# Optimization experiments

Measured on AMD Instinct MI355X. Metric: run time of the kernel, lower is better.

## Reference

```python
import jax, jax.numpy as jnp
import numpy as np

N = 4096
F_IN = 3000
F_OUT = 64
NEG_INF = jnp.float32(-9e15)


def _xavier(key, shape):
    fan_in, fan_out = shape[0], shape[-1]
    limit = (6.0 / (fan_in + fan_out)) ** 0.5
    return jax.random.uniform(key, shape, jnp.float32, -limit, limit)


def setup_inputs() -> dict:
    key = jax.random.key(0)
    ks = jax.random.split(key, 20)
    feat = jax.random.normal(ks[0], (N, F_IN), jnp.float32)
    feat_a = jax.random.normal(ks[1], (N, F_IN), jnp.float32)
    eye = jnp.eye(N, dtype=jnp.float32)
    adj = jnp.maximum((jax.random.uniform(ks[2], (N, N)) < 0.008).astype(jnp.float32), eye)
    graph_neigh = jnp.maximum((jax.random.uniform(ks[3], (N, N)) < 0.008).astype(jnp.float32), eye)
    return {
        "feat": feat,
        "feat_a": feat_a,
        "adj": adj,
        "graph_neigh": graph_neigh,
        "weight1": _xavier(ks[4], (F_IN, F_OUT)),
        "weight2": _xavier(ks[5], (F_OUT, F_IN)),
        "att_W": _xavier(ks[6], (F_OUT, F_OUT)),
        "a_src": _xavier(ks[7], (F_OUT, 1)),
        "a_dst": _xavier(ks[8], (F_OUT, 1)),
        "mlp_W1": _xavier(ks[9], (F_OUT, 256)),
        "mlp_b1": jnp.zeros((256,), jnp.float32),
        "mlp_W2": _xavier(ks[10], (256, 128)),
        "mlp_b2": jnp.zeros((128,), jnp.float32),
        "mlp_W3": _xavier(ks[11], (128, F_OUT)),
        "mlp_b3": jnp.zeros((F_OUT,), jnp.float32),
        "dmlp_W1": _xavier(ks[12], (F_OUT, 128)),
        "dmlp_b1": jnp.zeros((128,), jnp.float32),
        "dmlp_W2": _xavier(ks[13], (128, F_OUT)),
        "dmlp_b2": jnp.zeros((F_OUT,), jnp.float32),
        "bil_W": _xavier(ks[14], (F_OUT, F_OUT)),
        "bil_b": jnp.zeros((1,), jnp.float32),
    }


def reference(feat, feat_a, adj, graph_neigh,
              weight1, weight2, att_W, a_src, a_dst,
              mlp_W1, mlp_b1, mlp_W2, mlp_b2, mlp_W3, mlp_b3,
              dmlp_W1, dmlp_b1, dmlp_W2, dmlp_b2, bil_W, bil_b):
    relu = jax.nn.relu

    def attention(h):
        Wh = h @ att_W                      # [N, F_OUT]
        e = Wh @ a_src + (Wh @ a_dst).T     # [N, N]
        e = jnp.where(e > 0, e, 0.2 * e)    # LeakyReLU(0.2)
        e = jnp.where(adj > 0, e, NEG_INF)  # mask non-edges
        return jax.nn.softmax(e, axis=1) @ Wh

    def mlp(x):
        x = relu(x @ mlp_W1 + mlp_b1)
        x = relu(x @ mlp_W2 + mlp_b2)
        return x @ mlp_W3 + mlp_b3

    def dmlp(x):  # discriminator MLP: n_h -> 128 -> n_h
        return relu(x @ dmlp_W1 + dmlp_b1) @ dmlp_W2 + dmlp_b2

    def readout(emb):  # AvgReadout + L2 normalize
        g = (graph_neigh @ emb) / jnp.sum(graph_neigh, axis=1, keepdims=True)
        return g / jnp.maximum(jnp.linalg.norm(g, axis=1, keepdims=True), 1e-12)

    def bilinear(x, y):  # nn.Bilinear(n_h, n_h, 1)
        return (jnp.einsum('ni,ij,nj->n', x, bil_W, y) + bil_b)[:, None]

    def disc(c, h_pl, h_mi):
        c, h_pl, h_mi = dmlp(c), dmlp(h_pl), dmlp(h_mi)
        return jnp.concatenate([bilinear(h_pl, c), bilinear(h_mi, c)], axis=1)

    z = mlp(attention(feat @ weight1))
    hiden_emb = z
    h = adj @ (z @ weight2)                 # spmm(adj, z @ weight2)
    emb = relu(z)
    z_a = mlp(attention(feat_a @ weight1))
    emb_a = relu(z_a)
    g = jax.nn.sigmoid(readout(emb))
    g_a = jax.nn.sigmoid(readout(emb_a))
    ret = disc(g, emb, emb_a)
    ret_a = disc(g_a, emb_a, emb)
    return (hiden_emb, h, ret, ret_a)
```

## Files before the change

kernel.cpp:

```cpp
#include <hip/hip_runtime.h>

#define NN   4096
#define FIN  3000
#define MAXN 128

typedef unsigned short u16;
typedef __bf16 bf16x8 __attribute__((ext_vector_type(8)));
typedef float f32x16 __attribute__((ext_vector_type(16)));

__device__ __forceinline__ float bf2f(u16 u) { union { unsigned int i; float f; } v; v.i = ((unsigned int)u) << 16; return v.f; }
__device__ __forceinline__ u16 f2bf(float f) {
    union { float f; unsigned int i; } v; v.f = f;
    return (u16)((v.i + 0x7FFFu + ((v.i >> 16) & 1u)) >> 16);
}
__device__ __forceinline__ bf16x8 bzero8() {
    union { unsigned long long q[2]; bf16x8 v; } u; u.q[0] = 0ull; u.q[1] = 0ull; return u.v;
}
__device__ __forceinline__ f32x16 fzero16() {
    f32x16 v;
    #pragma unroll
    for (int i = 0; i < 16; i++) v[i] = 0.f;
    return v;
}

__global__ __launch_bounds__(1024) void k_detect(const u16* __restrict__ feat, int* __restrict__ flag)
{
    __shared__ int tot;
    if (threadIdx.x == 0) tot = 0;
    __syncthreads();
    int ins = 0;
    for (int i = threadIdx.x; i < 16384; i += 1024) {
        u16 u = feat[i];
        int e = (u >> 7) & 0xFF;
        if (u != 0 && (e < 90 || e > 160)) ins++;
    }
    atomicAdd(&tot, ins);
    __syncthreads();
    if (threadIdx.x == 0) *flag = (tot > 1024) ? 1 : 0;
}

__global__ __launch_bounds__(256) void k_convw(const int* __restrict__ flag,
    const void* s0, const void* s1, const void* s2, const void* s3,
    const void* s4, const void* s5, const void* s6, const void* s7,
    const void* s8, const void* s9, const void* s10, const void* s11,
    const void* s12, const void* s13, const void* s14, const void* s15,
    float* __restrict__ dst)
{
    const void* srcs[16] = {s0,s1,s2,s3,s4,s5,s6,s7,s8,s9,s10,s11,s12,s13,s14,s15};
    const int offs[16] = {0,192000,196096,196160,196224,212608,212864,245632,245760,253952,254016,262208,262336,270528,270592,274688};
    const int ns[16]   = {192000,4096,64,64,16384,256,32768,128,8192,64,8192,128,8192,64,4096,1};
    int seg = blockIdx.y;
    int i = blockIdx.x * 256 + threadIdx.x;
    if (i >= ns[seg]) return;
    float v = (*flag) ? ((const float*)srcs[seg])[i] : bf2f(((const u16*)srcs[seg])[i]);
    dst[offs[seg] + i] = v;
}

__global__ __launch_bounds__(256) void k_convw2t(const int* __restrict__ flag,
    const void* __restrict__ src, u16* __restrict__ WH, u16* __restrict__ WL)
{
    int i = blockIdx.x * 256 + threadIdx.x;
    if (i >= 3008 * 64) return;
    int n = i >> 6, k = i & 63;
    float v = 0.f;
    if (n < FIN)
        v = (*flag) ? ((const float*)src)[(size_t)k * FIN + n]
                    : bf2f(((const u16*)src)[(size_t)k * FIN + n]);
    u16 h = f2bf(v);
    float r = v - bf2f(h);
    WH[i] = h;
    WL[i] = f2bf(r);
}

__global__ __launch_bounds__(256) void k_convw1t(const int* __restrict__ flag,
    const void* __restrict__ w1src, u16* __restrict__ BtH, u16* __restrict__ BtL)
{
    int i = blockIdx.x * 256 + threadIdx.x;
    if (i >= 64 * 3008) return;
    int c = i / 3008, k = i - c * 3008;
    float v = 0.f;
    if (k < 3000)
        v = (*flag) ? ((const float*)w1src)[(size_t)k * 64 + c]
                    : bf2f(((const u16*)w1src)[(size_t)k * 64 + c]);
    u16 h = f2bf(v);
    float r = v - bf2f(h);
    BtH[(size_t)c * 3008 + k] = h;
    BtL[(size_t)c * 3008 + k] = f2bf(r);
}

__global__ __launch_bounds__(256) void k_build_csr(const int* __restrict__ flag,
    const void* __restrict__ Av, const void* __restrict__ Gv,
    int* __restrict__ aCnt, int* __restrict__ aIdx,
    int* __restrict__ gCnt, int* __restrict__ gIdx)
{
    bool isf = (*flag != 0);
    const void* M = blockIdx.y ? Gv : Av;
    int* cnt = blockIdx.y ? gCnt : aCnt;
    int* idx = blockIdx.y ? gIdx : aIdx;
    int row = blockIdx.x, t = threadIdx.x;
    int c0 = t * 16;
    unsigned int mask = 0; int my = 0;
    if (isf) {
        const float4* r = (const float4*)((const float*)M + (size_t)row * NN + c0);
        union { float4 q[4]; float f[16]; } u;
        u.q[0] = r[0]; u.q[1] = r[1]; u.q[2] = r[2]; u.q[3] = r[3];
        #pragma unroll
        for (int j = 0; j < 16; j++) if (u.f[j] != 0.f) { mask |= 1u << j; my++; }
    } else {
        const uint4* r = (const uint4*)((const u16*)M + (size_t)row * NN + c0);
        union { uint4 q[2]; u16 h[16]; } u;
        u.q[0] = r[0]; u.q[1] = r[1];
        #pragma unroll
        for (int j = 0; j < 16; j++) if (u.h[j] != 0) { mask |= 1u << j; my++; }
    }
    __shared__ int sc[256];
    sc[t] = my;
    __syncthreads();
    for (int d = 1; d < 256; d <<= 1) {
        int v = (t >= d) ? sc[t - d] : 0;
        __syncthreads();
        sc[t] += v;
        __syncthreads();
    }
    int pos = sc[t] - my;
    for (int j = 0; j < 16; j++) {
        if (mask & (1u << j)) {
            if (pos < MAXN) idx[(size_t)row * MAXN + pos] = c0 + j;
            pos++;
        }
    }
    if (t == 0) { int total = sc[255]; cnt[row] = (total < MAXN) ? total : MAXN; }
}

__global__ __launch_bounds__(512) void k_featgemm_mfma(const int* __restrict__ flag,
    const void* __restrict__ F0v, const void* __restrict__ F1v,
    const u16* __restrict__ BtH, float* __restrict__ X0, float* __restrict__ X1)
{
    if (*flag) return;
    const u16* F = (const u16*)(blockIdx.y ? F1v : F0v);
    float* X = blockIdx.y ? X1 : X0;
    int r0 = blockIdx.x * 32;
    int tid = threadIdx.x;
    int w  = tid >> 6;
    int l  = tid & 63;
    int lr = l & 31;
    int kg = l >> 5;
    const u16* arow = F   + (size_t)(r0 + lr) * FIN + kg * 8;
    const u16* b0p  = BtH + (size_t)lr * 3008 + kg * 8;
    const u16* b1p  = BtH + (size_t)(lr + 32) * 3008 + kg * 8;
    f32x16 acc0 = fzero16(), acc1 = fzero16();
    #pragma unroll 4
    for (int s = w; s < 188; s += 8) {
        int kk = s * 16;
        bf16x8 a;
        if (kk + kg * 8 < FIN) a = *(const bf16x8*)(arow + kk);
        else                   a = bzero8();
        bf16x8 b0 = *(const bf16x8*)(b0p + kk);
        bf16x8 b1 = *(const bf16x8*)(b1p + kk);
        acc0 = __builtin_amdgcn_mfma_f32_32x32x16_bf16(a, b0, acc0, 0, 0, 0);
        acc1 = __builtin_amdgcn_mfma_f32_32x32x16_bf16(a, b1, acc1, 0, 0, 0);
    }
    __shared__ float red[8][2048];
    float* rp = red[w];
    #pragma unroll
    for (int reg = 0; reg < 16; reg++) {
        int row = (reg & 3) + 8 * (reg >> 2) + 4 * kg;
        rp[row * 64 + lr] = acc0[reg];
    }
    #pragma unroll
    for (int reg = 0; reg < 16; reg++) {
        int row = (reg & 3) + 8 * (reg >> 2) + 4 * kg;
        rp[row * 64 + 32 + lr] = acc1[reg];
    }
    __syncthreads();
    for (int i = tid; i < 2048; i += 512) {
        float s0 = 0.f;
        #pragma unroll
        for (int j = 0; j < 8; j++) s0 += red[j][i];
        X[(size_t)r0 * 64 + i] = s0;
    }
}

__device__ __forceinline__ void fg_issue(
    const float* __restrict__ arow,
    const u16* __restrict__ b0h, const u16* __restrict__ b1h,
    const u16* __restrict__ b0l, const u16* __restrict__ b1l,
    int s, int kg,
    float4& A0, float4& A1, bf16x8& H0, bf16x8& H1, bf16x8& L0, bf16x8& L1)
{
    if (s < 188) {
        int kk = s * 16;
        if (kk + kg * 8 < FIN) {
            A0 = *(const float4*)(arow + kk);
            A1 = *(const float4*)(arow + kk + 4);
        } else {
            A0 = make_float4(0.f, 0.f, 0.f, 0.f);
            A1 = make_float4(0.f, 0.f, 0.f, 0.f);
        }
        H0 = *(const bf16x8*)(b0h + kk);
        H1 = *(const bf16x8*)(b1h + kk);
        L0 = *(const bf16x8*)(b0l + kk);
        L1 = *(const bf16x8*)(b1l + kk);
    } else {
        A0 = make_float4(0.f, 0.f, 0.f, 0.f);
        A1 = make_float4(0.f, 0.f, 0.f, 0.f);
        H0 = bzero8(); H1 = bzero8(); L0 = bzero8(); L1 = bzero8();
    }
}

__device__ __forceinline__ void fg_step(
    const float4& A0, const float4& A1,
    const bf16x8& H0, const bf16x8& H1, const bf16x8& L0, const bf16x8& L1,
    f32x16& acc0, f32x16& acc1)
{
    float av[8] = {A0.x, A0.y, A0.z, A0.w, A1.x, A1.y, A1.z, A1.w};
    bf16x8 ah, al;
    #pragma unroll
    for (int j = 0; j < 8; j++) {
        __bf16 hv = (__bf16)av[j];
        ah[j] = hv;
        al[j] = (__bf16)(av[j] - (float)hv);
    }
    acc0 = __builtin_amdgcn_mfma_f32_32x32x16_bf16(ah, H0, acc0, 0, 0, 0);
    acc0 = __builtin_amdgcn_mfma_f32_32x32x16_bf16(al, H0, acc0, 0, 0, 0);
    acc0 = __builtin_amdgcn_mfma_f32_32x32x16_bf16(ah, L0, acc0, 0, 0, 0);
    acc1 = __builtin_amdgcn_mfma_f32_32x32x16_bf16(ah, H1, acc1, 0, 0, 0);
    acc1 = __builtin_amdgcn_mfma_f32_32x32x16_bf16(al, H1, acc1, 0, 0, 0);
    acc1 = __builtin_amdgcn_mfma_f32_32x32x16_bf16(ah, L1, acc1, 0, 0, 0);
}

__global__ __launch_bounds__(512) void k_featgemm_mfma_f32(const int* __restrict__ flag,
    const void* __restrict__ F0v, const void* __restrict__ F1v,
    const u16* __restrict__ BtH, const u16* __restrict__ BtL,
    float* __restrict__ X0, float* __restrict__ X1)
{
    if (!*flag) return;
    const float* F = (const float*)(blockIdx.y ? F1v : F0v);
    float* X = blockIdx.y ? X1 : X0;
    int r0 = blockIdx.x * 32;
    int tid = threadIdx.x;
    int w  = tid >> 6;
    int l  = tid & 63;
    int lr = l & 31;
    int kg = l >> 5;
    int s0 = blockIdx.z * 8 + w;
    const float* arow = F + (size_t)(r0 + lr) * FIN + kg * 8;
    const u16* b0h = BtH + (size_t)lr * 3008 + kg * 8;
    const u16* b1h = BtH + (size_t)(lr + 32) * 3008 + kg * 8;
    const u16* b0l = BtL + (size_t)lr * 3008 + kg * 8;
    const u16* b1l = BtL + (size_t)(lr + 32) * 3008 + kg * 8;

    float4 A0[2], A1[2];
    bf16x8 H0[2], H1[2], L0[2], L1[2];
    fg_issue(arow, b0h, b1h, b0l, b1l, s0,      kg, A0[0], A1[0], H0[0], H1[0], L0[0], L1[0]);
    fg_issue(arow, b0h, b1h, b0l, b1l, s0 + 16, kg, A0[1], A1[1], H0[1], H1[1], L0[1], L1[1]);
    f32x16 acc0 = fzero16(), acc1 = fzero16();
    #pragma unroll
    for (int si = 0; si < 12; si++) {
        int sl = si & 1;
        fg_step(A0[sl], A1[sl], H0[sl], H1[sl], L0[sl], L1[sl], acc0, acc1);
        if (si + 2 < 12)
            fg_issue(arow, b0h, b1h, b0l, b1l, s0 + (si + 2) * 16, kg,
                     A0[sl], A1[sl], H0[sl], H1[sl], L0[sl], L1[sl]);
    }

    __shared__ float red[8][2048];
    float* rp = red[w];
    #pragma unroll
    for (int reg = 0; reg < 16; reg++) {
        int row = (reg & 3) + 8 * (reg >> 2) + 4 * kg;
        rp[row * 64 + lr] = acc0[reg];
    }
    #pragma unroll
    for (int reg = 0; reg < 16; reg++) {
        int row = (reg & 3) + 8 * (reg >> 2) + 4 * kg;
        rp[row * 64 + 32 + lr] = acc1[reg];
    }
    __syncthreads();
    for (int i = tid; i < 2048; i += 512) {
        float s0s = 0.f;
        #pragma unroll
        for (int j = 0; j < 8; j++) s0s += red[j][i];
        atomicAdd(&X[(size_t)r0 * 64 + i], s0s);
    }
}

__global__ __launch_bounds__(64) void k_whsd(
    const float* __restrict__ X1, const float* __restrict__ X2,
    const float* __restrict__ AW, const float* __restrict__ asrc, const float* __restrict__ adst,
    float* __restrict__ Wh1, float* __restrict__ Wh2,
    float* __restrict__ s1, float* __restrict__ s2,
    float* __restrict__ d1, float* __restrict__ d2)
{
    const float* X = blockIdx.y ? X2 : X1;
    float* Wh = blockIdx.y ? Wh2 : Wh1;
    float* sv = blockIdx.y ? s2 : s1;
    float* dv = blockIdx.y ? d2 : d1;
    int row = blockIdx.x, c = threadIdx.x;
    __shared__ float x[64];
    x[c] = X[(size_t)row * 64 + c];
    __syncthreads();
    float acc = 0.f;
    #pragma unroll 16
    for (int k = 0; k < 64; k++) acc += x[k] * AW[k * 64 + c];
    Wh[(size_t)row * 64 + c] = acc;
    float vs = acc * asrc[c];
    float vd = acc * adst[c];
    #pragma unroll
    for (int off = 32; off > 0; off >>= 1) { vs += __shfl_down(vs, off); vd += __shfl_down(vd, off); }
    if (c == 0) { sv[row] = vs; dv[row] = vd; }
}

__global__ __launch_bounds__(128) void k_attn(
    const int* __restrict__ cnt, const int* __restrict__ idx,
    const float* __restrict__ s1, const float* __restrict__ s2,
    const float* __restrict__ d1, const float* __restrict__ d2,
    const float* __restrict__ Wh1, const float* __restrict__ Wh2,
    float* __restrict__ A1, float* __restrict__ A2)
{
    const float* sp = blockIdx.y ? s2 : s1;
    const float* dp = blockIdx.y ? d2 : d1;
    const float* Wh = blockIdx.y ? Wh2 : Wh1;
    float* A = blockIdx.y ? A2 : A1;
    int row = blockIdx.x, tid = threadIdx.x;
    int n = cnt[row];
    __shared__ int js[MAXN];
    __shared__ float ps[MAXN];
    __shared__ float red2[2];
    __shared__ float ared[2][64];
    for (int k = tid; k < n; k += 128) js[k] = idx[(size_t)row * MAXN + k];
    __syncthreads();
    float si = sp[row];
    float m = -3.0e38f;
    for (int k = tid; k < n; k += 128) {
        float e = si + dp[js[k]];
        e = e > 0.f ? e : 0.2f * e;
        ps[k] = e;
        m = fmaxf(m, e);
    }
    #pragma unroll
    for (int off = 32; off > 0; off >>= 1) m = fmaxf(m, __shfl_down(m, off));
    if ((tid & 63) == 0) red2[tid >> 6] = m;
    __syncthreads();
    m = fmaxf(red2[0], red2[1]);
    __syncthreads();
    float zz = 0.f;
    for (int k = tid; k < n; k += 128) {
        float p = __expf(ps[k] - m);
        ps[k] = p;
        zz += p;
    }
    #pragma unroll
    for (int off = 32; off > 0; off >>= 1) zz += __shfl_down(zz, off);
    if ((tid & 63) == 0) red2[tid >> 6] = zz;
    __syncthreads();
    float Z = red2[0] + red2[1];
    Z = fmaxf(Z, 1e-20f);
    int f = tid & 63, half = tid >> 6;
    float acc = 0.f;
    for (int k = half; k < n; k += 2) acc += ps[k] * Wh[(size_t)js[k] * 64 + f];
    ared[half][f] = acc;
    __syncthreads();
    if (tid < 64) A[(size_t)row * 64 + f] = (ared[0][f] + ared[1][f]) / Z;
}

__global__ __launch_bounds__(256) void k_mlp(const int* __restrict__ flag,
    const float* __restrict__ A1, const float* __restrict__ A2,
    const float* __restrict__ W1, const float* __restrict__ b1,
    const float* __restrict__ W2, const float* __restrict__ b2,
    const float* __restrict__ W3, const float* __restrict__ b3,
    float* __restrict__ Z1, float* __restrict__ Z2, void* __restrict__ hidenv)
{
    const float* A = blockIdx.y ? A2 : A1;
    float* Z = blockIdx.y ? Z2 : Z1;
    int row0 = blockIdx.x * 4, tid = threadIdx.x;
    __shared__ float x[4][64], h1[4][256], h2[4][128];
    {
        int r = tid >> 6, c = tid & 63;
        x[r][c] = A[(size_t)(row0 + r) * 64 + c];
    }
    __syncthreads();
    {
        float a0 = b1[tid], a1v = a0, a2v = a0, a3v = a0;
        #pragma unroll 8
        for (int k = 0; k < 64; k++) {
            float w = W1[k * 256 + tid];
            a0 += x[0][k] * w; a1v += x[1][k] * w; a2v += x[2][k] * w; a3v += x[3][k] * w;
        }
        h1[0][tid] = fmaxf(a0, 0.f);  h1[1][tid] = fmaxf(a1v, 0.f);
        h1[2][tid] = fmaxf(a2v, 0.f); h1[3][tid] = fmaxf(a3v, 0.f);
    }
    __syncthreads();
    if (tid < 128) {
        float a0 = b2[tid], a1v = a0, a2v = a0, a3v = a0;
        #pragma unroll 8
        for (int k = 0; k < 256; k++) {
            float w = W2[k * 128 + tid];
            a0 += h1[0][k] * w; a1v += h1[1][k] * w; a2v += h1[2][k] * w; a3v += h1[3][k] * w;
        }
        h2[0][tid] = fmaxf(a0, 0.f);  h2[1][tid] = fmaxf(a1v, 0.f);
        h2[2][tid] = fmaxf(a2v, 0.f); h2[3][tid] = fmaxf(a3v, 0.f);
    }
    __syncthreads();
    if (tid < 64) {
        float a[4];
        a[0] = a[1] = a[2] = a[3] = b3[tid];
        #pragma unroll 8
        for (int k = 0; k < 128; k++) {
            float w = W3[k * 64 + tid];
            a[0] += h2[0][k] * w; a[1] += h2[1][k] * w; a[2] += h2[2][k] * w; a[3] += h2[3][k] * w;
        }
        bool isf = (*flag != 0);
        #pragma unroll
        for (int r = 0; r < 4; r++) {
            size_t ei = (size_t)(row0 + r) * 64 + tid;
            Z[ei] = a[r];
            if (blockIdx.y == 0) {
                if (isf) ((float*)hidenv)[ei] = a[r];
                else     ((u16*)hidenv)[ei] = f2bf(a[r]);
            }
        }
    }
}

__global__ __launch_bounds__(64) void k_spmm(
    const int* __restrict__ cnt, const int* __restrict__ idx,
    const float* __restrict__ Z, float* __restrict__ T)
{
    int row = blockIdx.x, f = threadIdx.x;
    int n = cnt[row];
    const int* ir = idx + (size_t)row * MAXN;
    float acc = 0.f;
    for (int k = 0; k < n; k++) acc += Z[(size_t)ir[k] * 64 + f];
    T[(size_t)row * 64 + f] = acc;
}

__global__ __launch_bounds__(256) void k_hgemm_mfma(const int* __restrict__ flag,
    const float* __restrict__ T, const u16* __restrict__ WH, const u16* __restrict__ WL,
    void* __restrict__ outv)
{
    bool isf = (*flag != 0);
    int tid = threadIdx.x;
    int w = tid >> 6, l = tid & 63, lr = l & 31, kg = l >> 5;
    int ct = blockIdx.y * 4 + w;
    if (ct >= 94) return;
    int r0 = blockIdx.x * 32, c0 = ct * 32;
    const float* tp = T + (size_t)(r0 + lr) * 64 + kg * 8;
    bf16x8 ah[4], al[4];
    #pragma unroll
    for (int s = 0; s < 4; s++) {
        float4 p0 = *(const float4*)(tp + s * 16);
        float4 p1 = *(const float4*)(tp + s * 16 + 4);
        float av[8] = {p0.x, p0.y, p0.z, p0.w, p1.x, p1.y, p1.z, p1.w};
        #pragma unroll
        for (int j = 0; j < 8; j++) {
            __bf16 hv = (__bf16)av[j];
            ah[s][j] = hv;
            al[s][j] = (__bf16)(av[j] - (float)hv);
        }
    }
    const u16* bh = WH + (size_t)(c0 + lr) * 64 + kg * 8;
    const u16* bl = WL + (size_t)(c0 + lr) * 64 + kg * 8;
    f32x16 acc = fzero16();
    #pragma unroll
    for (int s = 0; s < 4; s++) {
        bf16x8 vh = *(const bf16x8*)(bh + s * 16);
        bf16x8 vl = *(const bf16x8*)(bl + s * 16);
        acc = __builtin_amdgcn_mfma_f32_32x32x16_bf16(ah[s], vh, acc, 0, 0, 0);
        acc = __builtin_amdgcn_mfma_f32_32x32x16_bf16(al[s], vh, acc, 0, 0, 0);
        acc = __builtin_amdgcn_mfma_f32_32x32x16_bf16(ah[s], vl, acc, 0, 0, 0);
    }
    int col = c0 + lr;
    bool cok = col < FIN;
    #pragma unroll
    for (int reg = 0; reg < 16; reg++) {
        int row = (reg & 3) + 8 * (reg >> 2) + 4 * kg;
        size_t ei = 262144 + (size_t)(r0 + row) * FIN + col;
        if (cok) {
            if (isf) ((float*)outv)[ei] = acc[reg];
            else     ((u16*)outv)[ei] = f2bf(acc[reg]);
        }
    }
}

__global__ __launch_bounds__(64) void k_readout(
    const int* __restrict__ cnt, const int* __restrict__ idx,
    const float* __restrict__ Z1, const float* __restrict__ Z2,
    float* __restrict__ G1, float* __restrict__ G2)
{
    const float* Z = blockIdx.y ? Z2 : Z1;
    float* G = blockIdx.y ? G2 : G1;
    int row = blockIdx.x, f = threadIdx.x;
    int n = cnt[row];
    const int* ir = idx + (size_t)row * MAXN;
    float acc = 0.f;
    for (int k = 0; k < n; k++) acc += fmaxf(Z[(size_t)ir[k] * 64 + f], 0.f);
    acc /= (float)(n > 0 ? n : 1);
    float sq = acc * acc;
    #pragma unroll
    for (int off = 32; off > 0; off >>= 1) sq += __shfl_down(sq, off);
    sq = __shfl(sq, 0);
    float nrm = fmaxf(sqrtf(sq), 1e-12f);
    float v = acc / nrm;
    G[(size_t)row * 64 + f] = 1.f / (1.f + __expf(-v));
}

__global__ __launch_bounds__(128) void k_dmlp(
    const float* __restrict__ z, const float* __restrict__ za,
    const float* __restrict__ g, const float* __restrict__ ga,
    const float* __restrict__ W1, const float* __restrict__ b1,
    const float* __restrict__ W2, const float* __restrict__ b2,
    float* __restrict__ De, float* __restrict__ Dea,
    float* __restrict__ Dg, float* __restrict__ Dga)
{
    int w = blockIdx.y;
    const float* X = (w == 0) ? z : (w == 1) ? za : (w == 2) ? g : ga;
    float* O = (w == 0) ? De : (w == 1) ? Dea : (w == 2) ? Dg : Dga;
    int doRelu = (w < 2);
    int row0 = blockIdx.x * 4, tid = threadIdx.x;
    __shared__ float x[4][64], h1[4][128];
    for (int i = tid; i < 256; i += 128) {
        int r = i >> 6, c = i & 63;
        float v = X[(size_t)(row0 + r) * 64 + c];
        x[r][c] = doRelu ? fmaxf(v, 0.f) : v;
    }
    __syncthreads();
    {
        float a0 = b1[tid], a1v = a0, a2v = a0, a3v = a0;
        #pragma unroll 8
        for (int k = 0; k < 64; k++) {
            float w_ = W1[k * 128 + tid];
            a0 += x[0][k] * w_; a1v += x[1][k] * w_; a2v += x[2][k] * w_; a3v += x[3][k] * w_;
        }
        h1[0][tid] = fmaxf(a0, 0.f);  h1[1][tid] = fmaxf(a1v, 0.f);
        h1[2][tid] = fmaxf(a2v, 0.f); h1[3][tid] = fmaxf(a3v, 0.f);
    }
    __syncthreads();
    if (tid < 64) {
        float a[4];
        a[0] = a[1] = a[2] = a[3] = b2[tid];
        #pragma unroll 8
        for (int k = 0; k < 128; k++) {
            float w_ = W2[k * 64 + tid];
            a[0] += h1[0][k] * w_; a[1] += h1[1][k] * w_; a[2] += h1[2][k] * w_; a[3] += h1[3][k] * w_;
        }
        #pragma unroll
        for (int r = 0; r < 4; r++) O[(size_t)(row0 + r) * 64 + tid] = a[r];
    }
}

__global__ __launch_bounds__(64) void k_bilin(const int* __restrict__ flag,
    const float* __restrict__ De, const float* __restrict__ Dea,
    const float* __restrict__ Dg, const float* __restrict__ Dga,
    const float* __restrict__ BW, const float* __restrict__ bb, void* __restrict__ outv)
{
    int w = blockIdx.y;
    const float* X = (w == 0 || w == 3) ? De : Dea;
    const float* Y = (w <= 1) ? Dg : Dga;
    size_t bse = (w <= 1) ? (size_t)12550144 : (size_t)12558336;
    int col = (w == 0 || w == 2) ? 0 : 1;
    int row = blockIdx.x, k = threadIdx.x;
    __shared__ float x[64], y[64];
    x[k] = X[(size_t)row * 64 + k];
    y[k] = Y[(size_t)row * 64 + k];
    __syncthreads();
    float wv = 0.f;
    #pragma unroll 8
    for (int j = 0; j < 64; j++) wv += BW[k * 64 + j] * y[j];
    float v = x[k] * wv;
    #pragma unroll
    for (int off = 32; off > 0; off >>= 1) v += __shfl_down(v, off);
    if (k == 0) {
        float r = v + bb[0];
        size_t ei = bse + (size_t)row * 2 + col;
        if (*flag) ((float*)outv)[ei] = r;
        else       ((u16*)outv)[ei] = f2bf(r);
    }
}

extern "C" void kernel_launch(void* const* d_in, const int* in_sizes, int n_in,
                              void* d_out, int out_size, void* d_ws, size_t ws_size,
                              hipStream_t stream) {
    const void* feat   = d_in[0];
    const void* feat_a = d_in[1];
    const void* adj    = d_in[2];
    const void* gn     = d_in[3];
    const void* w1     = d_in[4];
    const void* w2     = d_in[5];
    const void* attW   = d_in[6];
    const void* a_src  = d_in[7];
    const void* a_dst  = d_in[8];
    const void* mW1    = d_in[9];
    const void* mb1    = d_in[10];
    const void* mW2    = d_in[11];
    const void* mb2    = d_in[12];
    const void* mW3    = d_in[13];
    const void* mb3    = d_in[14];
    const void* dW1    = d_in[15];
    const void* db1    = d_in[16];
    const void* dW2    = d_in[17];
    const void* db2    = d_in[18];
    const void* bW     = d_in[19];
    const void* bb     = d_in[20];
    (void)in_sizes; (void)n_in; (void)out_size;

    char* wsb = (char*)d_ws;
    int*   flag = (int*)wsb;
    float* T    = (float*)(wsb + 256);
    u16*   W2tH = (u16*)(wsb + 256 + 1048576);
    u16*   W2tL = W2tH + 3008 * 64;
    (void)ws_size;

    char* sc = (char*)d_out + 1048576;
    size_t soff = 0;
    auto salloc = [&](size_t nbytes) -> void* {
        void* p = (void*)(sc + soff);
        soff += (nbytes + 255) & ~(size_t)255;
        return p;
    };
    const size_t NV = (size_t)NN * 64;
    float* wA   = (float*)salloc((size_t)274689 * 4);
    int*   aCnt = (int*)salloc(NN * 4);
    int*   gCnt = (int*)salloc(NN * 4);
    int*   aIdx = (int*)salloc((size_t)NN * MAXN * 4);
    int*   gIdx = (int*)salloc((size_t)NN * MAXN * 4);
    float* X1  = (float*)salloc(NV * 4);
    float* X2  = (float*)salloc(NV * 4);
    float* Wh1 = (float*)salloc(NV * 4);
    float* Wh2 = (float*)salloc(NV * 4);
    float* A1  = (float*)salloc(NV * 4);
    float* A2  = (float*)salloc(NV * 4);
    float* z   = (float*)salloc(NV * 4);
    float* za  = (float*)salloc(NV * 4);
    float* g   = (float*)salloc(NV * 4);
    float* ga  = (float*)salloc(NV * 4);
    float* De  = (float*)salloc(NV * 4);
    float* Dea = (float*)salloc(NV * 4);
    float* Dg  = (float*)salloc(NV * 4);
    float* Dga = (float*)salloc(NV * 4);
    float* s1  = (float*)salloc(NN * 4);
    float* s2  = (float*)salloc(NN * 4);
    float* d1  = (float*)salloc(NN * 4);
    float* d2  = (float*)salloc(NN * 4);

    float* w1f   = wA + 0;
    float* attWf = wA + 192000;
    float* asrcf = wA + 196096;
    float* adstf = wA + 196160;
    float* mW1f  = wA + 196224;
    float* mb1f  = wA + 212608;
    float* mW2f  = wA + 212864;
    float* mb2f  = wA + 245632;
    float* mW3f  = wA + 245760;
    float* mb3f  = wA + 253952;
    float* dW1f  = wA + 254016;
    float* db1f  = wA + 262208;
    float* dW2f  = wA + 262336;
    float* db2f  = wA + 270528;
    float* bWf   = wA + 270592;
    float* bbf   = wA + 274688;

    u16* BtH = (u16*)De;
    u16* BtL = (u16*)Dea;

    k_detect<<<1, 1024, 0, stream>>>((const u16*)feat, flag);
    k_convw<<<dim3(750, 16), 256, 0, stream>>>(flag,
        w1, attW, a_src, a_dst, mW1, mb1, mW2, mb2, mW3, mb3,
        dW1, db1, dW2, db2, bW, bb, wA);
    k_convw2t<<<752, 256, 0, stream>>>(flag, w2, W2tH, W2tL);
    k_convw1t<<<752, 256, 0, stream>>>(flag, w1, BtH, BtL);
    k_build_csr<<<dim3(NN, 2), 256, 0, stream>>>(flag, adj, gn, aCnt, aIdx, gCnt, gIdx);
    hipMemsetAsync(X1, 0, 2 * NV * 4, stream);
    k_featgemm_mfma<<<dim3(NN / 32, 2), 512, 0, stream>>>(flag, feat, feat_a, BtH, X1, X2);
    k_featgemm_mfma_f32<<<dim3(NN / 32, 2, 2), 512, 0, stream>>>(flag, feat, feat_a, BtH, BtL, X1, X2);
    k_whsd<<<dim3(NN, 2), 64, 0, stream>>>(X1, X2, attWf, asrcf, adstf, Wh1, Wh2, s1, s2, d1, d2);
    k_attn<<<dim3(NN, 2), 128, 0, stream>>>(aCnt, aIdx, s1, s2, d1, d2, Wh1, Wh2, A1, A2);
    k_mlp<<<dim3(NN / 4, 2), 256, 0, stream>>>(flag, A1, A2, mW1f, mb1f, mW2f, mb2f, mW3f, mb3f, z, za, d_out);
    k_readout<<<dim3(NN, 2), 64, 0, stream>>>(gCnt, gIdx, z, za, g, ga);
    k_dmlp<<<dim3(NN / 4, 4), 128, 0, stream>>>(z, za, g, ga, dW1f, db1f, dW2f, db2f, De, Dea, Dg, Dga);
    k_bilin<<<dim3(NN, 4), 64, 0, stream>>>(flag, De, Dea, Dg, Dga, bWf, bbf, d_out);
    k_spmm<<<NN, 64, 0, stream>>>(aCnt, aIdx, z, T);
    k_hgemm_mfma<<<dim3(NN / 32, 24), 256, 0, stream>>>(flag, T, W2tH, W2tL, d_out);
}
```

Measured before the change: 469.0 us.

## Restructure fp32-split feature GEMM into contiguous K-chunks with direct atomic accumulation

The fp32-input feature GEMM now gives each wave its own 32-row tile over a contiguous 12-step K chunk, using 16 K-chunks per row block instead of strided steps across 8 waves. A triple-buffered prefetch replaces the double buffer, and the last chunk handles the K tail with bounds checks. The LDS cross-wave reduction and its barrier are removed; each wave atomically adds its accumulators straight to global memory. This frees 64KB of LDS, which should raise occupancy, but it issues far more global float atomics per output element.

Result: slower. 481.1 us (+2.6%).

```diff
diff --git a/kernel.cpp b/kernel.cpp
--- a/kernel.cpp
+++ b/kernel.cpp
@@ -181,33 +181,22 @@
     }
 }
 
-__device__ __forceinline__ void fg_issue(
-    const float* __restrict__ arow,
+__device__ __forceinline__ void fg_loadA(const float* __restrict__ arow, int kk,
+                                         float4& A0, float4& A1)
+{
+    A0 = *(const float4*)(arow + kk);
+    A1 = *(const float4*)(arow + kk + 4);
+}
+__device__ __forceinline__ void fg_loadB(
     const u16* __restrict__ b0h, const u16* __restrict__ b1h,
-    const u16* __restrict__ b0l, const u16* __restrict__ b1l,
-    int s, int kg,
-    float4& A0, float4& A1, bf16x8& H0, bf16x8& H1, bf16x8& L0, bf16x8& L1)
-{
-    if (s < 188) {
-        int kk = s * 16;
-        if (kk + kg * 8 < FIN) {
-            A0 = *(const float4*)(arow + kk);
-            A1 = *(const float4*)(arow + kk + 4);
-        } else {
-            A0 = make_float4(0.f, 0.f, 0.f, 0.f);
-            A1 = make_float4(0.f, 0.f, 0.f, 0.f);
-        }
-        H0 = *(const bf16x8*)(b0h + kk);
-        H1 = *(const bf16x8*)(b1h + kk);
-        L0 = *(const bf16x8*)(b0l + kk);
-        L1 = *(const bf16x8*)(b1l + kk);
-    } else {
-        A0 = make_float4(0.f, 0.f, 0.f, 0.f);
-        A1 = make_float4(0.f, 0.f, 0.f, 0.f);
-        H0 = bzero8(); H1 = bzero8(); L0 = bzero8(); L1 = bzero8();
-    }
-}
-
+    const u16* __restrict__ b0l, const u16* __restrict__ b1l, int kk,
+    bf16x8& H0, bf16x8& H1, bf16x8& L0, bf16x8& L1)
+{
+    H0 = *(const bf16x8*)(b0h + kk);
+    H1 = *(const bf16x8*)(b1h + kk);
+    L0 = *(const bf16x8*)(b0l + kk);
+    L1 = *(const bf16x8*)(b1l + kk);
+}
 __device__ __forceinline__ void fg_step(
     const float4& A0, const float4& A1,
     const bf16x8& H0, const bf16x8& H1, const bf16x8& L0, const bf16x8& L1,
@@ -229,7 +218,7 @@
     acc1 = __builtin_amdgcn_mfma_f32_32x32x16_bf16(ah, L1, acc1, 0, 0, 0);
 }
 
-__global__ __launch_bounds__(512) void k_featgemm_mfma_f32(const int* __restrict__ flag,
+__global__ __launch_bounds__(256) void k_featgemm_mfma_f32(const int* __restrict__ flag,
     const void* __restrict__ F0v, const void* __restrict__ F1v,
     const u16* __restrict__ BtH, const u16* __restrict__ BtL,
     float* __restrict__ X0, float* __restrict__ X1)
@@ -237,51 +226,61 @@
     if (!*flag) return;
     const float* F = (const float*)(blockIdx.y ? F1v : F0v);
     float* X = blockIdx.y ? X1 : X0;
-    int r0 = blockIdx.x * 32;
     int tid = threadIdx.x;
     int w  = tid >> 6;
     int l  = tid & 63;
     int lr = l & 31;
     int kg = l >> 5;
-    int s0 = blockIdx.z * 8 + w;
+    int r0 = blockIdx.x * 128 + w * 32;
+    int chunk = blockIdx.z;
     const float* arow = F + (size_t)(r0 + lr) * FIN + kg * 8;
     const u16* b0h = BtH + (size_t)lr * 3008 + kg * 8;
     const u16* b1h = BtH + (size_t)(lr + 32) * 3008 + kg * 8;
     const u16* b0l = BtL + (size_t)lr * 3008 + kg * 8;
     const u16* b1l = BtL + (size_t)(lr + 32) * 3008 + kg * 8;
-
-    float4 A0[2], A1[2];
-    bf16x8 H0[2], H1[2], L0[2], L1[2];
-    fg_issue(arow, b0h, b1h, b0l, b1l, s0,      kg, A0[0], A1[0], H0[0], H1[0], L0[0], L1[0]);
-    fg_issue(arow, b0h, b1h, b0l, b1l, s0 + 16, kg, A0[1], A1[1], H0[1], H1[1], L0[1], L1[1]);
     f32x16 acc0 = fzero16(), acc1 = fzero16();
-    #pragma unroll
-    for (int si = 0; si < 12; si++) {
-        int sl = si & 1;
-        fg_step(A0[sl], A1[sl], H0[sl], H1[sl], L0[sl], L1[sl], acc0, acc1);
-        if (si + 2 < 12)
-            fg_issue(arow, b0h, b1h, b0l, b1l, s0 + (si + 2) * 16, kg,
-                     A0[sl], A1[sl], H0[sl], H1[sl], L0[sl], L1[sl]);
-    }
-
-    __shared__ float red[8][2048];
-    float* rp = red[w];
+
+    if (chunk < 15) {
+        int sbase = chunk * 12;
+        float4 A0[3], A1[3];
+        bf16x8 H0[3], H1[3], L0[3], L1[3];
+        fg_loadA(arow, (sbase + 0) * 16, A0[0], A1[0]);
+        fg_loadB(b0h, b1h, b0l, b1l, (sbase + 0) * 16, H0[0], H1[0], L0[0], L1[0]);
+        fg_loadA(arow, (sbase + 1) * 16, A0[1], A1[1]);
+        fg_loadB(b0h, b1h, b0l, b1l, (sbase + 1) * 16, H0[1], H1[1], L0[1], L1[1]);
+        #pragma unroll
+        for (int j = 0; j < 12; j++) {
+            int cur = j % 3, nxt = (j + 2) % 3;
+            if (j < 10) {
+                int kk = (sbase + j + 2) * 16;
+                fg_loadA(arow, kk, A0[nxt], A1[nxt]);
+                fg_loadB(b0h, b1h, b0l, b1l, kk, H0[nxt], H1[nxt], L0[nxt], L1[nxt]);
+            }
+            fg_step(A0[cur], A1[cur], H0[cur], H1[cur], L0[cur], L1[cur], acc0, acc1);
+        }
+    } else {
+        for (int s = 180; s < 188; s++) {
+            int kk = s * 16;
+            float4 A0v, A1v;
+            if (kk + kg * 8 < FIN) {
+                A0v = *(const float4*)(arow + kk);
+                A1v = *(const float4*)(arow + kk + 4);
+            } else {
+                A0v = make_float4(0.f, 0.f, 0.f, 0.f);
+                A1v = make_float4(0.f, 0.f, 0.f, 0.f);
+            }
+            bf16x8 H0v, H1v, L0v, L1v;
+            fg_loadB(b0h, b1h, b0l, b1l, kk, H0v, H1v, L0v, L1v);
+            fg_step(A0v, A1v, H0v, H1v, L0v, L1v, acc0, acc1);
+        }
+    }
+
     #pragma unroll
     for (int reg = 0; reg < 16; reg++) {
         int row = (reg & 3) + 8 * (reg >> 2) + 4 * kg;
-        rp[row * 64 + lr] = acc0[reg];
-    }
-    #pragma unroll
-    for (int reg = 0; reg < 16; reg++) {
-        int row = (reg & 3) + 8 * (reg >> 2) + 4 * kg;
-        rp[row * 64 + 32 + lr] = acc1[reg];
-    }
-    __syncthreads();
-    for (int i = tid; i < 2048; i += 512) {
-        float s0s = 0.f;
-        #pragma unroll
-        for (int j = 0; j < 8; j++) s0s += red[j][i];
-        atomicAdd(&X[(size_t)r0 * 64 + i], s0s);
+        float* xp = X + (size_t)(r0 + row) * 64;
+        atomicAdd(xp + lr, acc0[reg]);
+        atomicAdd(xp + 32 + lr, acc1[reg]);
     }
 }
 
@@ -672,7 +671,7 @@
     k_build_csr<<<dim3(NN, 2), 256, 0, stream>>>(flag, adj, gn, aCnt, aIdx, gCnt, gIdx);
     hipMemsetAsync(X1, 0, 2 * NV * 4, stream);
     k_featgemm_mfma<<<dim3(NN / 32, 2), 512, 0, stream>>>(flag, feat, feat_a, BtH, X1, X2);
-    k_featgemm_mfma_f32<<<dim3(NN / 32, 2, 2), 512, 0, stream>>>(flag, feat, feat_a, BtH, BtL, X1, X2);
+    k_featgemm_mfma_f32<<<dim3(NN / 128, 2, 16), 256, 0, stream>>>(flag, feat, feat_a, BtH, BtL, X1, X2);
     k_whsd<<<dim3(NN, 2), 64, 0, stream>>>(X1, X2, attWf, asrcf, adstf, Wh1, Wh2, s1, s2, d1, d2);
     k_attn<<<dim3(NN, 2), 128, 0, stream>>>(aCnt, aIdx, s1, s2, d1, d2, Wh1, Wh2, A1, A2);
     k_mlp<<<dim3(NN / 4, 2), 256, 0, stream>>>(flag, A1, A2, mW1f, mb1f, mW2f, mb2f, mW3f, mb3f, z, za, d_out);
```
